# Kernel optimization log

Hardware: AMD Instinct MI355X
Metric: run time of the kernel (lower is better)

Reference implementation:

```python
import jax, jax.numpy as jnp
import numpy as np

C_IN = 512
OUT_CH = 256  # query/key gate channels
DIM = 64      # squeeze/extraction rank


def setup_inputs() -> dict:
    key = jax.random.key(0)
    ks = jax.random.split(key, 11)
    b, c, h, w = 16, C_IN, 64, 64

    def winit(k, o, i):
        # torch Conv2d default init: U(-s, s), s = 1/sqrt(fan_in)
        s = 1.0 / np.sqrt(i)
        return jax.random.uniform(k, (o, i), jnp.float32, -s, s)

    return {
        "x": jax.random.normal(ks[0], (b, c, h, w), jnp.float32),
        "Wq": winit(ks[1], OUT_CH, C_IN), "bq": winit(ks[2], OUT_CH, C_IN)[:, 0],
        "Wk": winit(ks[3], OUT_CH, C_IN), "bk": winit(ks[4], OUT_CH, C_IN)[:, 0],
        "Wv": winit(ks[5], C_IN, C_IN),   "bv": winit(ks[6], C_IN, C_IN)[:, 0],
        "Ws": winit(ks[7], DIM, C_IN),    "bs": winit(ks[8], DIM, C_IN)[:, 0],
        "We": winit(ks[9], DIM, C_IN),    "be": winit(ks[10], DIM, C_IN)[:, 0],
    }


def reference(x, Wq, bq, Wk, bk, Wv, bv, Ws, bs, We, be):
    b, c, h, w = x.shape
    n = h * w
    xf = x.reshape(b, c, n)  # [b, 512, n] (1x1 conv == matmul over channels)

    Q = jnp.einsum('oc,bcn->bon', Wq, xf) + bq[:, None]   # [b, 256, n]
    K = jnp.einsum('oc,bcn->bon', Wk, xf) + bk[:, None]   # [b, 256, n]
    gate = jax.nn.sigmoid(jnp.mean(Q * K, axis=1, keepdims=True))  # [b, 1, n]

    V = jnp.einsum('oc,bcn->bon', Wv, xf) + bv[:, None]   # [b, 512, n]
    V_dw = V * gate                                        # [b, 512, n]

    Qs = jnp.einsum('oc,bcn->bon', Ws, xf) + bs[:, None]   # [b, 64, n]
    Ke = jnp.einsum('oc,bcn->bon', We, xf) + be[:, None]   # [b, 64, n]

    energy = jnp.einsum('bcn,bdn->bcd', V_dw, Qs)           # [b, 512, 64]
    attention = jax.nn.softmax(energy, axis=-1)
    Vout = jnp.einsum('bcd,bdn->bcn', attention, Ke)        # [b, 512, n]

    return x + Vout.reshape(b, c, h, w)
```

## Files before the change

kernel.cpp:

```cpp
#include <hip/hip_runtime.h>

#define BATCH 16
#define CIN 512
#define NPIX 4096

typedef __attribute__((ext_vector_type(8))) short bf16x8;
typedef __attribute__((ext_vector_type(4))) float f32x4;

#define MFMA(a,b,c) __builtin_amdgcn_mfma_f32_16x16x32_bf16((a),(b),(c),0,0,0)

#define GLOAD(g, l) __builtin_amdgcn_global_load_lds( \
    (const __attribute__((address_space(1))) unsigned int*)(g), \
    (__attribute__((address_space(3))) unsigned int*)(l), 16, 0, 0)

union PK  { short s[8]; bf16x8 v; };
union PK4 { short s[4]; uint2 u; };

__device__ __forceinline__ unsigned short bf16_rne(float f){
  unsigned u = __float_as_uint(f);
  return (unsigned short)((u + 0x7fffu + ((u >> 16) & 1u)) >> 16);
}
__device__ __forceinline__ void f32_split(float f, short &h, short &l){
  unsigned short hu = bf16_rne(f);
  h = (short)hu;
  float fh = __uint_as_float((unsigned)hu << 16);
  l = (short)bf16_rne(f - fh);
}
__device__ __forceinline__ void split8(float4 a, float4 b, bf16x8 &h, bf16x8 &l){
  float vv[8] = {a.x,a.y,a.z,a.w,b.x,b.y,b.z,b.w};
  PK ph, pl;
  #pragma unroll
  for (int z=0;z<8;z++){ short hh,ll; f32_split(vv[z],hh,ll); ph.s[z]=hh; pl.s[z]=ll; }
  h = ph.v; l = pl.v;
}

__device__ __forceinline__ int offBig(int row, int k){
  int s = k >> 3;
  s = (s & ~7) | ((s ^ row) & 7);
  return row*512 + s*8 + (k & 7);
}

__global__ __launch_bounds__(256)
void k_convw(const float* __restrict__ Wq, const float* __restrict__ bq,
             const float* __restrict__ Wk, const float* __restrict__ bk,
             const float* __restrict__ Ws, const float* __restrict__ bs,
             const float* __restrict__ We, const float* __restrict__ be,
             short* __restrict__ WALL, short* __restrict__ WLOT,
             float* __restrict__ BG, float* __restrict__ BSE){
  int t = blockIdx.x*256 + threadIdx.x;
  if (t < 640*512){
    int r = t >> 9, k = t & 511;
    float v = (r < 512) ? ((r & 1) ? Wk[(r>>1)*512 + k] : Wq[(r>>1)*512 + k])
            : (r < 576) ? Ws[(r-512)*512 + k] : We[(r-576)*512 + k];
    short h, l; f32_split(v, h, l);
    int kt = k >> 5, lc = (k >> 3) & 3, e = k & 7;
    int pc = lc ^ (r & 3);
    WALL[((size_t)kt*640 + r)*32 + pc*8 + e] = h;
    if (r >= 512 && r < 576){
      int rlo = r - 512;
      WLOT[((size_t)kt*64 + rlo)*32 + (lc ^ (rlo & 3))*8 + e] = l;
    }
  }
  if (t < 512) BG[t] = (t & 1) ? bk[t>>1] : bq[t>>1];
  if (t < 128) BSE[t] = (t < 64) ? bs[t] : be[t-64];
}

__global__ __launch_bounds__(256)
void k_stage(const float* __restrict__ x, short* __restrict__ XT){
  __shared__ float XF[64*65];
  int cb = blockIdx.x, nb = blockIdx.y, b = blockIdx.z;
  int tid = threadIdx.x;
  {
    int cc = tid >> 2, ni = (tid & 3) * 16;
    const float* xp = x + ((size_t)(b*CIN + cb*64 + cc))*NPIX + nb*64 + ni;
    #pragma unroll
    for (int u=0;u<16;u+=4){
      float4 v = *(const float4*)(xp + u);
      XF[cc*65 + ni+u+0] = v.x; XF[cc*65 + ni+u+1] = v.y;
      XF[cc*65 + ni+u+2] = v.z; XF[cc*65 + ni+u+3] = v.w;
    }
  }
  __syncthreads();
  {
    int nn = tid & 63, cg = (tid >> 6) * 16;
    PK c0, c1;
    #pragma unroll
    for (int i=0;i<8;i++) c0.s[i] = (short)bf16_rne(XF[(cg+i)*65 + nn]);
    #pragma unroll
    for (int i=0;i<8;i++) c1.s[i] = (short)bf16_rne(XF[(cg+8+i)*65 + nn]);
    short* dst = XT + ((size_t)(b*64 + nb))*64*512;
    int ch0 = cb*8 + (cg>>3), ch1 = ch0 + 1;
    int s0 = (ch0 & ~7) | ((ch0 ^ nn) & 7);
    int s1 = (ch1 & ~7) | ((ch1 ^ nn) & 7);
    *(bf16x8*)&dst[nn*512 + s0*8] = c0.v;
    *(bf16x8*)&dst[nn*512 + s1*8] = c1.v;
  }
}

__global__ __launch_bounds__(512)
void k_gemm(const short* __restrict__ XT, const short* __restrict__ WALL,
            const short* __restrict__ WLOT, const float* __restrict__ BG,
            const float* __restrict__ BSE,
            float* __restrict__ QSG, short* __restrict__ KET, float* __restrict__ S){
  __shared__ __align__(16) short XS[64*512];
  float* QKf = (float*)XS;
  float* GF  = ((float*)XS) + 512;
  int nt = blockIdx.x, b = blockIdx.y;
  int n0 = nt*64;
  int tid = threadIdx.x, w = tid>>6, lane = tid&63;
  int lr = lane&15, lk = (lane>>4)<<3;
  int cg = lane>>4;

  {
    const char* src = (const char*)(XT + ((size_t)(b*64 + nt))*64*512);
    char* dstbase = (char*)XS;
    #pragma unroll
    for (int i=0;i<8;i++)
      GLOAD(src + i*8192 + tid*16, dstbase + i*8192 + (tid & ~63)*16);
  }
  __syncthreads();

  f32x4 acc[5][4] = {};
  int rowBase = w*80;
  int swz = ((cg ^ (lr & 3)) << 3);

  for (int kt=0; kt<16; kt++){
    bf16x8 bb[4];
    #pragma unroll
    for (int j=0;j<4;j++)
      bb[j] = *(const bf16x8*)&XS[offBig(j*16+lr, kt*32+lk)];
    const short* wk = WALL + (size_t)kt*640*32;
    #pragma unroll
    for (int r=0;r<5;r++){
      int rowL = rowBase + r*16 + lr;
      bf16x8 a = *(const bf16x8*)&wk[rowL*32 + swz];
      #pragma unroll
      for (int j=0;j<4;j++) acc[r][j] = MFMA(a, bb[j], acc[r][j]);
      int F = w*5 + r;
      if (F >= 32 && F < 36){
        bf16x8 alo = *(const bf16x8*)&WLOT[(size_t)kt*64*32 + (F*16-512+lr)*32 + swz];
        #pragma unroll
        for (int j=0;j<4;j++) acc[r][j] = MFMA(alo, bb[j], acc[r][j]);
      }
    }
  }
  __syncthreads();

  int rq = (lane>>4)<<2;
  {
    float p[4] = {0.f,0.f,0.f,0.f};
    #pragma unroll
    for (int r=0;r<5;r++){
      int F = w*5 + r;
      if (F < 32){
        f32x4 bg = *(const f32x4*)&BG[F*16 + rq];
        #pragma unroll
        for (int j=0;j<4;j++){
          f32x4 a4 = acc[r][j];
          p[j] += (a4[0]+bg[0])*(a4[1]+bg[1]) + (a4[2]+bg[2])*(a4[3]+bg[3]);
        }
      }
    }
    #pragma unroll
    for (int j=0;j<4;j++){ p[j] += __shfl_xor(p[j],16); p[j] += __shfl_xor(p[j],32); }
    if (lane < 16){
      #pragma unroll
      for (int j=0;j<4;j++) QKf[w*64 + j*16 + lane] = p[j];
    }
  }
  __syncthreads();
  if (tid < 64){
    float s = 0.f;
    #pragma unroll
    for (int ww=0;ww<8;ww++) s += QKf[ww*64 + tid];
    GF[tid] = 1.f/(1.f + __expf(-s*(1.f/256.f)));
  }
  __syncthreads();

  #pragma unroll
  for (int r=0;r<5;r++){
    int F = w*5 + r;
    if (F >= 32 && F < 36){
      int row0 = F*16 - 512 + rq;
      f32x4 bs4 = *(const f32x4*)&BSE[row0];
      float srow[4] = {0.f,0.f,0.f,0.f};
      #pragma unroll
      for (int j=0;j<4;j++){
        int nl = j*16 + lr;
        float g = GF[nl];
        int n = n0 + nl;
        #pragma unroll
        for (int q=0;q<4;q++){
          float v = (acc[r][j][q] + bs4[q]) * g;
          QSG[((size_t)(b*64) + row0 + q)*NPIX + n] = v;
          srow[q] += v;
        }
      }
      #pragma unroll
      for (int q=0;q<4;q++){
        float v = srow[q];
        v += __shfl_xor(v,1); v += __shfl_xor(v,2);
        v += __shfl_xor(v,4); v += __shfl_xor(v,8);
        if (lr == 0) atomicAdd(&S[b*64 + row0 + q], v);
      }
    } else if (F >= 36){
      int d0 = F*16 - 576 + rq;
      f32x4 be4 = *(const f32x4*)&BSE[64 + d0];
      #pragma unroll
      for (int j=0;j<4;j++){
        int n = n0 + j*16 + lr;
        PK4 pk;
        #pragma unroll
        for (int q=0;q<4;q++) pk.s[q] = (short)bf16_rne(acc[r][j][q] + be4[q]);
        *(uint2*)&KET[((size_t)(b*NPIX) + n)*64 + d0] = pk.u;
      }
    }
  }
}

__global__ __launch_bounds__(512)
void k_M(const float* __restrict__ x, const float* __restrict__ QSG,
         float* __restrict__ M){
  int slab = blockIdx.x, b = blockIdx.y;
  int tid = threadIdx.x, w = tid>>6, lane = tid&63;
  int lr = lane&15, lk8 = (lane>>4)<<3;
  f32x4 acc[4][4] = {};
  for (int kt=0; kt<8; kt++){
    int noff = slab*256 + kt*32 + lk8;
    bf16x8 bh[4], bl[4];
    #pragma unroll
    for (int j=0;j<4;j++){
      const float* qp = QSG + ((size_t)(b*64) + j*16 + lr)*NPIX + noff;
      split8(*(const float4*)qp, *(const float4*)(qp+4), bh[j], bl[j]);
    }
    #pragma unroll
    for (int r=0;r<4;r++){
      const float* xp = x + ((size_t)(b*CIN) + w*64 + r*16 + lr)*NPIX + noff;
      bf16x8 ah, al;
      split8(*(const float4*)xp, *(const float4*)(xp+4), ah, al);
      #pragma unroll
      for (int j=0;j<4;j++){
        acc[r][j] = MFMA(al, bh[j], acc[r][j]);
        acc[r][j] = MFMA(ah, bl[j], acc[r][j]);
        acc[r][j] = MFMA(ah, bh[j], acc[r][j]);
      }
    }
  }
  int rq = (lane>>4)<<2;
  #pragma unroll
  for (int r=0;r<4;r++)
    #pragma unroll
    for (int j=0;j<4;j++)
      #pragma unroll
      for (int q=0;q<4;q++)
        atomicAdd(&M[((size_t)(b*CIN) + w*64 + r*16 + rq + q)*64 + j*16 + lr], acc[r][j][q]);
}

__global__ __launch_bounds__(256)
void k_energy(const float* __restrict__ Wv, const float* __restrict__ bv,
              const float* __restrict__ M, const float* __restrict__ S,
              float* __restrict__ EN){
  __shared__ __align__(16) float ML[128*68];
  int cch = blockIdx.x, b = blockIdx.y;
  int tid = threadIdx.x;
  int d4 = tid & 15, ci = tid >> 4;
  f32x4 acc[2] = {};
  for (int kt=0; kt<4; kt++){
    __syncthreads();
    for (int i = tid; i < 2048; i += 256){
      int k = i >> 4, c4 = (i & 15) * 4;
      *(float4*)&ML[k*68 + c4] = *(const float4*)&M[((size_t)(b*CIN) + kt*128 + k)*64 + c4];
    }
    __syncthreads();
    #pragma unroll
    for (int m=0;m<2;m++){
      int c = cch*32 + ci + 16*m;
      const float* wvp = Wv + (size_t)c*512 + kt*128;
      for (int k4=0;k4<32;k4++){
        float4 wv4 = *(const float4*)(wvp + k4*4);
        f32x4 m0 = *(const f32x4*)&ML[(k4*4+0)*68 + d4*4];
        f32x4 m1 = *(const f32x4*)&ML[(k4*4+1)*68 + d4*4];
        f32x4 m2 = *(const f32x4*)&ML[(k4*4+2)*68 + d4*4];
        f32x4 m3 = *(const f32x4*)&ML[(k4*4+3)*68 + d4*4];
        acc[m] += m0*wv4.x + m1*wv4.y + m2*wv4.z + m3*wv4.w;
      }
    }
  }
  f32x4 s4 = *(const f32x4*)&S[b*64 + d4*4];
  #pragma unroll
  for (int m=0;m<2;m++){
    int c = cch*32 + ci + 16*m;
    f32x4 r = acc[m] + s4*bv[c];
    *(f32x4*)&EN[((size_t)(b*CIN) + c)*64 + d4*4] = r;
  }
}

__global__ __launch_bounds__(256)
void k_softmax(const float* __restrict__ EN, short* __restrict__ ATT){
  int row = blockIdx.x*4 + (threadIdx.x>>6);
  int lane = threadIdx.x & 63;
  float v = EN[(size_t)row*64 + lane];
  float m = v;
  #pragma unroll
  for (int s=1;s<64;s<<=1) m = fmaxf(m, __shfl_xor(m, s));
  float e = __expf(v - m);
  float sum = e;
  #pragma unroll
  for (int s=1;s<64;s<<=1) sum += __shfl_xor(sum, s);
  ATT[(size_t)row*64 + lane] = (short)bf16_rne(e / sum);
}

__global__ __launch_bounds__(512)
void k_out(const float* __restrict__ x, const short* __restrict__ ATT,
           const short* __restrict__ KET, float* __restrict__ out){
  int nt = blockIdx.x, b = blockIdx.y;
  int n0 = nt*64;
  int tid = threadIdx.x, w = tid>>6, lane = tid&63;
  int lr = lane&15, lk = (lane>>4)<<3;
  f32x4 acc[4][4] = {};
  #pragma unroll
  for (int kt=0; kt<2; kt++){
    bf16x8 bb[4];
    #pragma unroll
    for (int j=0;j<4;j++)
      bb[j] = *(const bf16x8*)&KET[((size_t)(b*NPIX) + n0 + j*16 + lr)*64 + kt*32 + lk];
    #pragma unroll
    for (int r=0;r<4;r++){
      bf16x8 a = *(const bf16x8*)&ATT[((size_t)(b*CIN) + w*64 + r*16 + lr)*64 + kt*32 + lk];
      #pragma unroll
      for (int j=0;j<4;j++)
        acc[r][j] = MFMA(a, bb[j], acc[r][j]);
    }
  }
  int rq = (lane>>4)<<2;
  #pragma unroll
  for (int r=0;r<4;r++)
    #pragma unroll
    for (int j=0;j<4;j++){
      int col = n0 + j*16 + lr;
      #pragma unroll
      for (int q=0;q<4;q++){
        size_t idx = ((size_t)(b*CIN) + w*64 + r*16 + rq + q)*NPIX + col;
        out[idx] = x[idx] + acc[r][j][q];
      }
    }
}

extern "C" void kernel_launch(void* const* d_in, const int* in_sizes, int n_in,
                              void* d_out, int out_size, void* d_ws, size_t ws_size,
                              hipStream_t stream){
  const float* x   = (const float*)d_in[0];
  const float* Wq  = (const float*)d_in[1];
  const float* bq  = (const float*)d_in[2];
  const float* Wk  = (const float*)d_in[3];
  const float* bk  = (const float*)d_in[4];
  const float* Wv  = (const float*)d_in[5];
  const float* bv  = (const float*)d_in[6];
  const float* Wsq = (const float*)d_in[7];
  const float* bsq = (const float*)d_in[8];
  const float* We  = (const float*)d_in[9];
  const float* be  = (const float*)d_in[10];
  float* out = (float*)d_out;

  char* wsb = (char*)d_ws;
  size_t off = 0;
  auto alloc = [&](size_t bytes)->void*{
    void* p = wsb + off; off += (bytes + 255) & ~(size_t)255; return p;
  };
  short* WALL = (short*)alloc((size_t)640*512*2);
  short* WLOT = (short*)alloc((size_t)64*512*2);
  float* BG   = (float*)alloc(512*4);
  float* BSE  = (float*)alloc(128*4);
  short* XT   = (short*)alloc((size_t)BATCH*NPIX*512*2);
  float* QSG  = (float*)alloc((size_t)BATCH*64*NPIX*4);
  short* KET  = (short*)alloc((size_t)BATCH*NPIX*64*2);
  float* Mb   = (float*)alloc((size_t)BATCH*512*64*4);
  float* Sb   = (float*)alloc((size_t)BATCH*64*4);
  float* EN   = (float*)alloc((size_t)BATCH*512*64*4);
  short* ATT  = (short*)alloc((size_t)BATCH*512*64*2);

  hipMemsetAsync(Mb, 0, (size_t)BATCH*512*64*4, stream);
  hipMemsetAsync(Sb, 0, (size_t)BATCH*64*4, stream);

  k_convw  <<<1280, 256, 0, stream>>>(Wq,bq,Wk,bk,Wsq,bsq,We,be, WALL,WLOT,BG,BSE);
  k_stage  <<<dim3(8,64,16), 256, 0, stream>>>(x, XT);
  k_gemm   <<<dim3(64,16), 512, 0, stream>>>(XT, WALL, WLOT, BG, BSE, QSG, KET, Sb);
  k_M      <<<dim3(16,16), 512, 0, stream>>>(x, QSG, Mb);
  k_energy <<<dim3(16,16), 256, 0, stream>>>(Wv, bv, Mb, Sb, EN);
  k_softmax<<<2048, 256, 0, stream>>>(EN, ATT);
  k_out    <<<dim3(64,16), 512, 0, stream>>>(x, ATT, KET, out);
}
```

Measured before the change: 310.9 us.

## Split fused projection GEMM into tiled double-buffered gate and Qs/Ke GEMMs

Replaces the single per-64-pixel GEMM, which held the whole 64x512 X tile in LDS and streamed weights from global memory, with two 128x128-tiled GEMM kernels that double-buffer A and B k-slices in LDS through global_load_lds. The Q·K bias cross terms are folded algebraically into a precomputed vector VV dotted with x during staging, plus a scalar DD, so the gate GEMM skips the per-element bias adds. The low part of the split-precision Ws weights becomes extra rows of the weight matrix instead of a separate MFMA pass. This raises parallelism and data reuse, at the cost of an extra gate kernel, an extra memset, and global atomics for the QK partial sums.

```diff
diff --git a/kernel.cpp b/kernel.cpp
--- a/kernel.cpp
+++ b/kernel.cpp
@@ -34,39 +34,50 @@
   h = ph.v; l = pl.v;
 }
 
-__device__ __forceinline__ int offBig(int row, int k){
-  int s = k >> 3;
-  s = (s & ~7) | ((s ^ row) & 7);
-  return row*512 + s*8 + (k & 7);
-}
-
 __global__ __launch_bounds__(256)
 void k_convw(const float* __restrict__ Wq, const float* __restrict__ bq,
              const float* __restrict__ Wk, const float* __restrict__ bk,
              const float* __restrict__ Ws, const float* __restrict__ bs,
              const float* __restrict__ We, const float* __restrict__ be,
-             short* __restrict__ WALL, short* __restrict__ WLOT,
-             float* __restrict__ BG, float* __restrict__ BSE){
+             short* __restrict__ WALL2, float* __restrict__ BSE,
+             float* __restrict__ VV, float* __restrict__ DD){
   int t = blockIdx.x*256 + threadIdx.x;
-  if (t < 640*512){
+  if (t < 768*512){
     int r = t >> 9, k = t & 511;
-    float v = (r < 512) ? ((r & 1) ? Wk[(r>>1)*512 + k] : Wq[(r>>1)*512 + k])
-            : (r < 576) ? Ws[(r-512)*512 + k] : We[(r-576)*512 + k];
-    short h, l; f32_split(v, h, l);
+    float v;
+    short out;
+    if (r < 512){
+      v = (r & 1) ? Wk[(r>>1)*512 + k] : Wq[(r>>1)*512 + k];
+      out = (short)bf16_rne(v);
+    } else if (r < 576){
+      short h,l; f32_split(Ws[(r-512)*512 + k], h, l); out = h;
+    } else if (r < 640){
+      short h,l; f32_split(Ws[(r-576)*512 + k], h, l); out = l;
+    } else if (r < 704){
+      out = (short)bf16_rne(We[(r-640)*512 + k]);
+    } else {
+      out = 0;
+    }
     int kt = k >> 5, lc = (k >> 3) & 3, e = k & 7;
     int pc = lc ^ (r & 3);
-    WALL[((size_t)kt*640 + r)*32 + pc*8 + e] = h;
-    if (r >= 512 && r < 576){
-      int rlo = r - 512;
-      WLOT[((size_t)kt*64 + rlo)*32 + (lc ^ (rlo & 3))*8 + e] = l;
-    }
-  }
-  if (t < 512) BG[t] = (t & 1) ? bk[t>>1] : bq[t>>1];
+    WALL2[((size_t)kt*768 + r)*32 + pc*8 + e] = out;
+  }
   if (t < 128) BSE[t] = (t < 64) ? bs[t] : be[t-64];
-}
-
-__global__ __launch_bounds__(256)
-void k_stage(const float* __restrict__ x, short* __restrict__ XT){
+  if (t < 512){
+    float a = 0.f;
+    for (int o=0;o<256;o++) a += bq[o]*Wk[o*512+t] + bk[o]*Wq[o*512+t];
+    VV[t] = a;
+  }
+  if (t == 0){
+    float a = 0.f;
+    for (int o=0;o<256;o++) a += bq[o]*bk[o];
+    DD[0] = a;
+  }
+}
+
+__global__ __launch_bounds__(256)
+void k_stage(const float* __restrict__ x, const float* __restrict__ VV,
+             short* __restrict__ XT2, float* __restrict__ QKacc){
   __shared__ float XF[64*65];
   int cb = blockIdx.x, nb = blockIdx.y, b = blockIdx.z;
   int tid = threadIdx.x;
@@ -82,137 +93,206 @@
   }
   __syncthreads();
   {
-    int nn = tid & 63, cg = (tid >> 6) * 16;
+    int nn = tid >> 2, cs = tid & 3;
+    int nl = (nb & 1)*64 + nn, nt = nb >> 1;
+    int kt = cb*2 + (cs >> 1);
+    float pa = 0.f;
     PK c0, c1;
     #pragma unroll
-    for (int i=0;i<8;i++) c0.s[i] = (short)bf16_rne(XF[(cg+i)*65 + nn]);
-    #pragma unroll
-    for (int i=0;i<8;i++) c1.s[i] = (short)bf16_rne(XF[(cg+8+i)*65 + nn]);
-    short* dst = XT + ((size_t)(b*64 + nb))*64*512;
-    int ch0 = cb*8 + (cg>>3), ch1 = ch0 + 1;
-    int s0 = (ch0 & ~7) | ((ch0 ^ nn) & 7);
-    int s1 = (ch1 & ~7) | ((ch1 ^ nn) & 7);
-    *(bf16x8*)&dst[nn*512 + s0*8] = c0.v;
-    *(bf16x8*)&dst[nn*512 + s1*8] = c1.v;
-  }
-}
-
-__global__ __launch_bounds__(512)
-void k_gemm(const short* __restrict__ XT, const short* __restrict__ WALL,
-            const short* __restrict__ WLOT, const float* __restrict__ BG,
-            const float* __restrict__ BSE,
-            float* __restrict__ QSG, short* __restrict__ KET, float* __restrict__ S){
-  __shared__ __align__(16) short XS[64*512];
-  float* QKf = (float*)XS;
-  float* GF  = ((float*)XS) + 512;
-  int nt = blockIdx.x, b = blockIdx.y;
-  int n0 = nt*64;
+    for (int i=0;i<8;i++){
+      float f = XF[(cs*16 + i)*65 + nn];
+      pa += VV[cb*64 + cs*16 + i] * f;
+      c0.s[i] = (short)bf16_rne(f);
+    }
+    #pragma unroll
+    for (int i=0;i<8;i++){
+      float f = XF[(cs*16 + 8 + i)*65 + nn];
+      pa += VV[cb*64 + cs*16 + 8 + i] * f;
+      c1.s[i] = (short)bf16_rne(f);
+    }
+    short* rowb = XT2 + ((((size_t)(b*32 + nt))*16 + kt)*128 + nl)*32;
+    int pc0 = ((cs & 1)*2 + 0) ^ (nl & 3);
+    int pc1 = ((cs & 1)*2 + 1) ^ (nl & 3);
+    *(bf16x8*)&rowb[pc0*8] = c0.v;
+    *(bf16x8*)&rowb[pc1*8] = c1.v;
+    pa += __shfl_xor(pa, 1);
+    pa += __shfl_xor(pa, 2);
+    if ((tid & 3) == 0)
+      atomicAdd(&QKacc[(size_t)b*NPIX + nb*64 + nn], pa);
+  }
+}
+
+__global__ __launch_bounds__(256)
+void k_gemm1(const short* __restrict__ WALL2, const short* __restrict__ XT2,
+             float* __restrict__ QKacc){
+  __shared__ __align__(16) char SMEM[32768];
+  short (*As)[128*32] = (short(*)[128*32])SMEM;
+  short (*Bs)[128*32] = (short(*)[128*32])(SMEM + 16384);
+  __shared__ float QKp[2][2][4][16];
+  int nt = blockIdx.x, mt = blockIdx.y, b = blockIdx.z;
   int tid = threadIdx.x, w = tid>>6, lane = tid&63;
-  int lr = lane&15, lk = (lane>>4)<<3;
-  int cg = lane>>4;
-
-  {
-    const char* src = (const char*)(XT + ((size_t)(b*64 + nt))*64*512);
-    char* dstbase = (char*)XS;
-    #pragma unroll
-    for (int i=0;i<8;i++)
-      GLOAD(src + i*8192 + tid*16, dstbase + i*8192 + (tid & ~63)*16);
+  int lr = lane&15, cg = lane>>4;
+  int rh = w>>1, nh = w&1;
+  const char* Abase = (const char*)WALL2 + (size_t)mt*128*64;
+  const char* Bbase = (const char*)XT2 + ((size_t)(b*32 + nt)*16)*8192;
+  #pragma unroll
+  for (int i=0;i<2;i++){
+    GLOAD(Abase + (i*256+tid)*16, ((char*)&As[0][0]) + (i*256+(tid&~63))*16);
+    GLOAD(Bbase + (i*256+tid)*16, ((char*)&Bs[0][0]) + (i*256+(tid&~63))*16);
+  }
+  f32x4 acc[4][4] = {};
+  int swz = ((cg ^ (lr&3)) << 3);
+  for (int kt=0; kt<16; kt++){
+    int cur = kt & 1;
+    __syncthreads();
+    if (kt < 15){
+      const char* An = Abase + (size_t)(kt+1)*768*64;
+      const char* Bn = Bbase + (size_t)(kt+1)*8192;
+      #pragma unroll
+      for (int i=0;i<2;i++){
+        GLOAD(An + (i*256+tid)*16, ((char*)&As[cur^1][0]) + (i*256+(tid&~63))*16);
+        GLOAD(Bn + (i*256+tid)*16, ((char*)&Bs[cur^1][0]) + (i*256+(tid&~63))*16);
+      }
+    }
+    bf16x8 a[4], bb[4];
+    #pragma unroll
+    for (int m=0;m<4;m++) a[m] = *(const bf16x8*)&As[cur][(rh*64 + m*16 + lr)*32 + swz];
+    #pragma unroll
+    for (int j=0;j<4;j++) bb[j] = *(const bf16x8*)&Bs[cur][(nh*64 + j*16 + lr)*32 + swz];
+    #pragma unroll
+    for (int m=0;m<4;m++)
+      #pragma unroll
+      for (int j=0;j<4;j++)
+        acc[m][j] = MFMA(a[m], bb[j], acc[m][j]);
+  }
+  float p[4] = {0.f,0.f,0.f,0.f};
+  #pragma unroll
+  for (int m=0;m<4;m++)
+    #pragma unroll
+    for (int j=0;j<4;j++){
+      f32x4 a4 = acc[m][j];
+      p[j] += a4[0]*a4[1] + a4[2]*a4[3];
+    }
+  #pragma unroll
+  for (int j=0;j<4;j++){ p[j] += __shfl_xor(p[j],16); p[j] += __shfl_xor(p[j],32); }
+  if (lane < 16){
+    #pragma unroll
+    for (int j=0;j<4;j++) QKp[rh][nh][j][lane] = p[j];
   }
   __syncthreads();
-
-  f32x4 acc[5][4] = {};
-  int rowBase = w*80;
-  int swz = ((cg ^ (lr & 3)) << 3);
-
+  if (rh == 0 && lane < 16){
+    #pragma unroll
+    for (int j=0;j<4;j++){
+      float v = QKp[0][nh][j][lane] + QKp[1][nh][j][lane];
+      atomicAdd(&QKacc[(size_t)b*NPIX + nt*128 + nh*64 + j*16 + lane], v);
+    }
+  }
+}
+
+__global__ __launch_bounds__(256)
+void k_gate(const float* __restrict__ QKacc, const float* __restrict__ DD,
+            float* __restrict__ GATE){
+  int i = blockIdx.x*256 + threadIdx.x;
+  GATE[i] = 1.f/(1.f + __expf(-(QKacc[i] + DD[0]) * (1.f/256.f)));
+}
+
+__global__ __launch_bounds__(256)
+void k_gemm2(const short* __restrict__ WALL2, const short* __restrict__ XT2,
+             const float* __restrict__ BSE, const float* __restrict__ GATE,
+             float* __restrict__ QSG, short* __restrict__ KET, float* __restrict__ S){
+  __shared__ __align__(16) char SMEM[32768];
+  short (*As)[128*32] = (short(*)[128*32])SMEM;
+  short (*Bs)[128*32] = (short(*)[128*32])(SMEM + 16384);
+  int nt = blockIdx.x, mt2 = blockIdx.y, b = blockIdx.z;
+  int tid = threadIdx.x, w = tid>>6, lane = tid&63;
+  int lr = lane&15, cg = lane>>4;
+  int rh = w>>1, nh = w&1;
+  const char* Abase = (const char*)WALL2 + (size_t)(512 + mt2*128)*64;
+  const char* Bbase = (const char*)XT2 + ((size_t)(b*32 + nt)*16)*8192;
+  #pragma unroll
+  for (int i=0;i<2;i++){
+    GLOAD(Abase + (i*256+tid)*16, ((char*)&As[0][0]) + (i*256+(tid&~63))*16);
+    GLOAD(Bbase + (i*256+tid)*16, ((char*)&Bs[0][0]) + (i*256+(tid&~63))*16);
+  }
+  f32x4 acc[4][4] = {};
+  int swz = ((cg ^ (lr&3)) << 3);
   for (int kt=0; kt<16; kt++){
-    bf16x8 bb[4];
-    #pragma unroll
-    for (int j=0;j<4;j++)
-      bb[j] = *(const bf16x8*)&XS[offBig(j*16+lr, kt*32+lk)];
-    const short* wk = WALL + (size_t)kt*640*32;
-    #pragma unroll
-    for (int r=0;r<5;r++){
-      int rowL = rowBase + r*16 + lr;
-      bf16x8 a = *(const bf16x8*)&wk[rowL*32 + swz];
-      #pragma unroll
-      for (int j=0;j<4;j++) acc[r][j] = MFMA(a, bb[j], acc[r][j]);
-      int F = w*5 + r;
-      if (F >= 32 && F < 36){
-        bf16x8 alo = *(const bf16x8*)&WLOT[(size_t)kt*64*32 + (F*16-512+lr)*32 + swz];
+    int cur = kt & 1;
+    __syncthreads();
+    if (kt < 15){
+      const char* An = Abase + (size_t)(kt+1)*768*64;
+      const char* Bn = Bbase + (size_t)(kt+1)*8192;
+      #pragma unroll
+      for (int i=0;i<2;i++){
+        GLOAD(An + (i*256+tid)*16, ((char*)&As[cur^1][0]) + (i*256+(tid&~63))*16);
+        GLOAD(Bn + (i*256+tid)*16, ((char*)&Bs[cur^1][0]) + (i*256+(tid&~63))*16);
+      }
+    }
+    bf16x8 a[4], bb[4];
+    #pragma unroll
+    for (int m=0;m<4;m++) a[m] = *(const bf16x8*)&As[cur][(rh*64 + m*16 + lr)*32 + swz];
+    #pragma unroll
+    for (int j=0;j<4;j++) bb[j] = *(const bf16x8*)&Bs[cur][(nh*64 + j*16 + lr)*32 + swz];
+    #pragma unroll
+    for (int m=0;m<4;m++)
+      #pragma unroll
+      for (int j=0;j<4;j++)
+        acc[m][j] = MFMA(a[m], bb[j], acc[m][j]);
+  }
+  __syncthreads();
+  int rq = (lane>>4)<<2;
+  if (mt2 == 0){
+    float* LO = (float*)SMEM;
+    if (rh == 1){
+      #pragma unroll
+      for (int m=0;m<4;m++)
         #pragma unroll
-        for (int j=0;j<4;j++) acc[r][j] = MFMA(alo, bb[j], acc[r][j]);
-      }
-    }
-  }
-  __syncthreads();
-
-  int rq = (lane>>4)<<2;
-  {
-    float p[4] = {0.f,0.f,0.f,0.f};
-    #pragma unroll
-    for (int r=0;r<5;r++){
-      int F = w*5 + r;
-      if (F < 32){
-        f32x4 bg = *(const f32x4*)&BG[F*16 + rq];
+        for (int j=0;j<4;j++)
+          #pragma unroll
+          for (int q=0;q<4;q++)
+            LO[nh*4096 + (m*16 + rq + q)*64 + j*16 + lr] = acc[m][j][q];
+    }
+    __syncthreads();
+    if (rh == 0){
+      #pragma unroll
+      for (int m=0;m<4;m++){
+        int o0 = m*16 + rq;
+        f32x4 bs4 = *(const f32x4*)&BSE[o0];
+        float srow[4] = {0.f,0.f,0.f,0.f};
         #pragma unroll
         for (int j=0;j<4;j++){
-          f32x4 a4 = acc[r][j];
-          p[j] += (a4[0]+bg[0])*(a4[1]+bg[1]) + (a4[2]+bg[2])*(a4[3]+bg[3]);
+          int n = nt*128 + nh*64 + j*16 + lr;
+          float g = GATE[(size_t)b*NPIX + n];
+          #pragma unroll
+          for (int q=0;q<4;q++){
+            float v = (acc[m][j][q] + LO[nh*4096 + (o0+q)*64 + j*16 + lr] + bs4[q]) * g;
+            QSG[((size_t)(b*64) + o0 + q)*NPIX + n] = v;
+            srow[q] += v;
+          }
         }
-      }
-    }
-    #pragma unroll
-    for (int j=0;j<4;j++){ p[j] += __shfl_xor(p[j],16); p[j] += __shfl_xor(p[j],32); }
-    if (lane < 16){
-      #pragma unroll
-      for (int j=0;j<4;j++) QKf[w*64 + j*16 + lane] = p[j];
-    }
-  }
-  __syncthreads();
-  if (tid < 64){
-    float s = 0.f;
-    #pragma unroll
-    for (int ww=0;ww<8;ww++) s += QKf[ww*64 + tid];
-    GF[tid] = 1.f/(1.f + __expf(-s*(1.f/256.f)));
-  }
-  __syncthreads();
-
-  #pragma unroll
-  for (int r=0;r<5;r++){
-    int F = w*5 + r;
-    if (F >= 32 && F < 36){
-      int row0 = F*16 - 512 + rq;
-      f32x4 bs4 = *(const f32x4*)&BSE[row0];
-      float srow[4] = {0.f,0.f,0.f,0.f};
-      #pragma unroll
-      for (int j=0;j<4;j++){
-        int nl = j*16 + lr;
-        float g = GF[nl];
-        int n = n0 + nl;
         #pragma unroll
         for (int q=0;q<4;q++){
-          float v = (acc[r][j][q] + bs4[q]) * g;
-          QSG[((size_t)(b*64) + row0 + q)*NPIX + n] = v;
-          srow[q] += v;
+          float v = srow[q];
+          v += __shfl_xor(v,1); v += __shfl_xor(v,2);
+          v += __shfl_xor(v,4); v += __shfl_xor(v,8);
+          if (lr == 0) atomicAdd(&S[b*64 + o0 + q], v);
         }
       }
-      #pragma unroll
-      for (int q=0;q<4;q++){
-        float v = srow[q];
-        v += __shfl_xor(v,1); v += __shfl_xor(v,2);
-        v += __shfl_xor(v,4); v += __shfl_xor(v,8);
-        if (lr == 0) atomicAdd(&S[b*64 + row0 + q], v);
-      }
-    } else if (F >= 36){
-      int d0 = F*16 - 576 + rq;
-      f32x4 be4 = *(const f32x4*)&BSE[64 + d0];
-      #pragma unroll
-      for (int j=0;j<4;j++){
-        int n = n0 + j*16 + lr;
-        PK4 pk;
+    }
+  } else {
+    if (rh == 0){
+      #pragma unroll
+      for (int m=0;m<4;m++){
+        int d0 = m*16 + rq;
+        f32x4 be4 = *(const f32x4*)&BSE[64 + d0];
         #pragma unroll
-        for (int q=0;q<4;q++) pk.s[q] = (short)bf16_rne(acc[r][j][q] + be4[q]);
-        *(uint2*)&KET[((size_t)(b*NPIX) + n)*64 + d0] = pk.u;
+        for (int j=0;j<4;j++){
+          int n = nt*128 + nh*64 + j*16 + lr;
+          PK4 pk;
+          #pragma unroll
+          for (int q=0;q<4;q++) pk.s[q] = (short)bf16_rne(acc[m][j][q] + be4[q]);
+          *(uint2*)&KET[((size_t)(b*NPIX) + n)*64 + d0] = pk.u;
+        }
       }
     }
   }
@@ -367,11 +447,13 @@
   auto alloc = [&](size_t bytes)->void*{
     void* p = wsb + off; off += (bytes + 255) & ~(size_t)255; return p;
   };
-  short* WALL = (short*)alloc((size_t)640*512*2);
-  short* WLOT = (short*)alloc((size_t)64*512*2);
-  float* BG   = (float*)alloc(512*4);
+  short* WALL2= (short*)alloc((size_t)768*512*2);
   float* BSE  = (float*)alloc(128*4);
-  short* XT   = (short*)alloc((size_t)BATCH*NPIX*512*2);
+  float* VV   = (float*)alloc(512*4);
+  float* DD   = (float*)alloc(256);
+  short* XT2  = (short*)alloc((size_t)BATCH*NPIX*512*2);
+  float* QKacc= (float*)alloc((size_t)BATCH*NPIX*4);
+  float* GATE = (float*)alloc((size_t)BATCH*NPIX*4);
   float* QSG  = (float*)alloc((size_t)BATCH*64*NPIX*4);
   short* KET  = (short*)alloc((size_t)BATCH*NPIX*64*2);
   float* Mb   = (float*)alloc((size_t)BATCH*512*64*4);
@@ -379,12 +461,15 @@
   float* EN   = (float*)alloc((size_t)BATCH*512*64*4);
   short* ATT  = (short*)alloc((size_t)BATCH*512*64*2);
 
+  hipMemsetAsync(QKacc, 0, (size_t)BATCH*NPIX*4, stream);
   hipMemsetAsync(Mb, 0, (size_t)BATCH*512*64*4, stream);
   hipMemsetAsync(Sb, 0, (size_t)BATCH*64*4, stream);
 
-  k_convw  <<<1280, 256, 0, stream>>>(Wq,bq,Wk,bk,Wsq,bsq,We,be, WALL,WLOT,BG,BSE);
-  k_stage  <<<dim3(8,64,16), 256, 0, stream>>>(x, XT);
-  k_gemm   <<<dim3(64,16), 512, 0, stream>>>(XT, WALL, WLOT, BG, BSE, QSG, KET, Sb);
+  k_convw  <<<1536, 256, 0, stream>>>(Wq,bq,Wk,bk,Wsq,bsq,We,be, WALL2,BSE,VV,DD);
+  k_stage  <<<dim3(8,64,16), 256, 0, stream>>>(x, VV, XT2, QKacc);
+  k_gemm1  <<<dim3(32,4,16), 256, 0, stream>>>(WALL2, XT2, QKacc);
+  k_gate   <<<256, 256, 0, stream>>>(QKacc, DD, GATE);
+  k_gemm2  <<<dim3(32,2,16), 256, 0, stream>>>(WALL2, XT2, BSE, GATE, QSG, KET, Sb);
   k_M      <<<dim3(16,16), 512, 0, stream>>>(x, QSG, Mb);
   k_energy <<<dim3(16,16), 256, 0, stream>>>(Wv, bv, Mb, Sb, EN);
   k_softmax<<<2048, 256, 0, stream>>>(EN, ATT);
```

Result: faster. 282.2 us (-9.2%).
